# Performance work log

Measured on AMD Instinct MI355X. Metric: run time of the kernel, lower is better.

Reference implementation:

```python
import jax, jax.numpy as jnp
import numpy as np

CLASH_WEIGHT = 0.05
PHYSICS_WEIGHT = 0.3
CLAMP_DIST = 10.0
EPS = 1e-8
C_IDX, N_IDX = 0, 1  # ATOM_TYPE_MAP['C'], ATOM_TYPE_MAP['N']


def setup_inputs() -> dict:
    key = jax.random.key(0)
    ks = jax.random.split(key, 8)
    B, R, A = 2, 1024, 4096
    return {
        'rots_pred': jax.random.normal(ks[0], (B, R, 3, 3), dtype=jnp.float32),
        'trans_pred': jax.random.normal(ks[1], (B, R, 3), dtype=jnp.float32),
        'coords_pred': jax.random.normal(ks[2], (B, A, 3), dtype=jnp.float32),
        'rots_true': jax.random.normal(ks[3], (B, R, 3, 3), dtype=jnp.float32),
        'trans_true': jax.random.normal(ks[4], (B, R, 3), dtype=jnp.float32),
        'coords_true': jax.random.normal(ks[5], (B, A, 3), dtype=jnp.float32),
        'atom_types': jax.random.randint(ks[6], (B, A), 0, 19, dtype=jnp.int32),
        'vdw_radii': jax.random.uniform(ks[7], (19,), dtype=jnp.float32),
        'res_mask': jnp.ones((B, R), dtype=jnp.float32),
        'mask': jnp.ones((B, A), dtype=jnp.float32),
    }


def _local_coords(rots, trans, coords):
    # invert_frames: R^-1 = R^T, t^-1 = -R^T t ; apply to all points per frame
    inv_rots = jnp.swapaxes(rots, -1, -2)                      # [B,R,3,3]
    inv_trans = -jnp.einsum('brij,brj->bri', inv_rots, trans)  # [B,R,3]
    # [B, R, A, 3]
    return jnp.einsum('brij,baj->brai', inv_rots, coords) + inv_trans[:, :, None, :]


def _pairwise_dist(coords, eps2=1e-12):
    # numerically-stable cdist via squared-norm expansion
    sq = jnp.sum(coords * coords, axis=-1)                      # [B,A]
    d2 = sq[:, :, None] + sq[:, None, :] - 2.0 * jnp.einsum('bad,bcd->bac', coords, coords)
    return jnp.sqrt(jnp.maximum(d2, eps2))                      # [B,A,A]


def reference(rots_pred, trans_pred, coords_pred, rots_true, trans_true,
              coords_true, atom_types, vdw_radii, res_mask, mask):
    # ---- FAPE ----
    lp = _local_coords(rots_pred, trans_pred, coords_pred)   # [B,R,A,3]
    lt = _local_coords(rots_true, trans_true, coords_true)   # [B,R,A,3]
    err = jnp.sqrt(jnp.sum((lp - lt) ** 2, axis=-1) + EPS)   # [B,R,A]
    err = jnp.minimum(err, CLAMP_DIST)
    err = err * mask[:, None, :] * res_mask[:, :, None]
    fape = jnp.sum(err) / (jnp.sum(mask) * jnp.sum(res_mask) + EPS)

    # shared pairwise distances on predicted coords
    d = _pairwise_dist(coords_pred)                          # [B,A,A]

    # ---- Clash ----
    radii = vdw_radii[atom_types]                            # [B,A]
    min_d = radii[:, :, None] + radii[:, None, :]
    clashes = (d < min_d) & (d > EPS)
    num_clashes = jnp.sum(clashes.astype(jnp.float32), axis=(-1, -2)) / 2.0
    num_atoms = coords_pred.shape[-2]
    clash = jnp.mean(num_clashes / num_atoms)

    # ---- Physics (C-N peptide bond length) ----
    is_c = atom_types == C_IDX
    is_n = atom_types == N_IDX
    cn_mask = (is_c[:, :, None] & is_n[:, None, :]).astype(jnp.float32)
    penalty = jax.nn.relu(jnp.abs(d - 1.33) - 0.2) * cn_mask
    total_pen = jnp.sum(penalty, axis=(-1, -2))
    n_pairs = jnp.maximum(jnp.sum(cn_mask, axis=(-1, -2)), 1.0)
    physics = jnp.mean(total_pen / n_pairs)

    total = fape + CLASH_WEIGHT * clash + PHYSICS_WEIGHT * physics
    return total
```

## Files before the change

kernel.cpp:

```cpp
#include <hip/hip_runtime.h>


constexpr int BB = 2;
constexpr int FR = 4;
constexpr int NI = 4;
constexpr int TJ = 16;
constexpr int IC = 1024;

constexpr int NB_FAPE = 512;
constexpr int NB_BAND = 512;
constexpr int NB_FULL = 768;
constexpr int NB_PAIR = NB_BAND + NB_FULL;

__device__ __forceinline__ float wred(float v) {
#pragma unroll
  for (int o = 32; o > 0; o >>= 1) v += __shfl_down(v, o, 64);
  return v;
}
__device__ __forceinline__ double wredd(double v) {
#pragma unroll
  for (int o = 32; o > 0; o >>= 1) v += __shfl_down(v, o, 64);
  return v;
}

template <bool BAND>
__device__ __forceinline__ void pair_body(
    const float* __restrict__ coords, const int* __restrict__ types,
    const float* __restrict__ vdw, int A, int b, int ic, int jt, int tid,
    float& out_clash, float& out_pen) {
  const int ibase = ic * IC;
  float xi[NI], yi[NI], zi[NI], qi[NI], ri[NI], cf[NI], nf[NI];
  int ii[NI];
#pragma unroll
  for (int k = 0; k < NI; ++k) {
    ii[k] = ibase + (k << 8) + tid;
    const size_t g = (size_t)b * A + ii[k];
    const float x = coords[g * 3], y = coords[g * 3 + 1], z = coords[g * 3 + 2];
    const int t = types[g];
    xi[k] = x; yi[k] = y; zi[k] = z;
    qi[k] = __fadd_rn(__fadd_rn(__fmul_rn(x, x), __fmul_rn(y, y)), __fmul_rn(z, z));
    ri[k] = vdw[t];
    cf[k] = (t == 0) ? 1.f : 0.f;
    nf[k] = (t == 1) ? 1.f : 0.f;
  }

  int cnt2 = 0, cnt1 = 0;
  float pen = 0.f;
  const int j0 = jt * TJ;
#pragma unroll 4
  for (int jj = 0; jj < TJ; ++jj) {
    const int j = j0 + jj;
    const size_t jg = (size_t)b * A + j;
    const float sx = coords[jg * 3], sy = coords[jg * 3 + 1], sz = coords[jg * 3 + 2];
    const int st = types[jg];
    const float sr = vdw[st];
    const float sq = __fadd_rn(__fadd_rn(__fmul_rn(sx, sx), __fmul_rn(sy, sy)),
                               __fmul_rn(sz, sz));
    float dsq[NI];
#pragma unroll
    for (int k = 0; k < NI; ++k) {
      const float dot = fmaf(zi[k], sz, fmaf(yi[k], sy, xi[k] * sx));
      float d2 = fmaf(-2.f, dot, qi[k] + sq);
      d2 = fmaxf(d2, 1e-12f);
      dsq[k] = d2;
      const float mind = ri[k] + sr;
      const bool c = d2 < mind * mind;
      if (BAND) {
        cnt2 += (c && (ii[k] < j)) ? 1 : 0;
        cnt1 += (c && (ii[k] == j)) ? 1 : 0;
      } else {
        cnt2 += c ? 1 : 0;
      }
    }
    if (st <= 1) {
      if (st == 1) {
#pragma unroll
        for (int k = 0; k < NI; ++k) {
          const float dd = __builtin_amdgcn_sqrtf(dsq[k]);
          float pp = fmaxf(fabsf(dd - 1.33f) - 0.2f, 0.f);
          if (BAND) pp = (ii[k] < j) ? pp : 0.f;
          pen = fmaf(pp, cf[k], pen);
        }
      } else {
#pragma unroll
        for (int k = 0; k < NI; ++k) {
          const float dd = __builtin_amdgcn_sqrtf(dsq[k]);
          float pp = fmaxf(fabsf(dd - 1.33f) - 0.2f, 0.f);
          if (BAND) pp = (ii[k] < j) ? pp : 0.f;
          pen = fmaf(pp, nf[k], pen);
        }
      }
    }
  }
  out_clash = 2.f * cnt2 + (float)cnt1;
  out_pen = pen;
}

__global__ __launch_bounds__(256) void fat_kernel(
    const float* __restrict__ rots_p, const float* __restrict__ trans_p,
    const float* __restrict__ coords_p,
    const float* __restrict__ rots_t, const float* __restrict__ trans_t,
    const float* __restrict__ coords_t,
    const int* __restrict__ types, const float* __restrict__ vdw,
    const float* __restrict__ res_mask, const float* __restrict__ mask,
    float* __restrict__ fape_part, float* __restrict__ clash_part,
    float* __restrict__ pen_part, int R, int A) {
  const int tid = threadIdx.x;
  const int bid = blockIdx.x;
  __shared__ float red[2][4];

  if (bid < NB_FAPE) {
    const int bpb = R / FR;
    const int b = bid / bpb;
    const int r0 = (bid % bpb) * FR;

    float rp[FR][9], rt[FR][9], cc[FR][3], rm[FR];
#pragma unroll
    for (int f = 0; f < FR; ++f) {
      const size_t fr = (size_t)(b * R + r0 + f);
      const float* Rp = rots_p + fr * 9;
      const float* Rt = rots_t + fr * 9;
      const float* Tp = trans_p + fr * 3;
      const float* Tt = trans_t + fr * 3;
#pragma unroll
      for (int k = 0; k < 9; ++k) { rp[f][k] = Rp[k]; rt[f][k] = Rt[k]; }
      const float tp0 = Tp[0], tp1 = Tp[1], tp2 = Tp[2];
      const float tt0 = Tt[0], tt1 = Tt[1], tt2 = Tt[2];
#pragma unroll
      for (int i = 0; i < 3; ++i) {
        cc[f][i] = (rp[f][0 + i] * tp0 + rp[f][3 + i] * tp1 + rp[f][6 + i] * tp2)
                 - (rt[f][0 + i] * tt0 + rt[f][3 + i] * tt1 + rt[f][6 + i] * tt2);
      }
      rm[f] = res_mask[fr];
    }

    float facc[FR];
#pragma unroll
    for (int f = 0; f < FR; ++f) facc[f] = 0.f;

    for (int a = tid; a < A; a += 256) {
      const size_t g = (size_t)b * A + a;
      const float x0 = coords_p[g * 3], x1 = coords_p[g * 3 + 1], x2 = coords_p[g * 3 + 2];
      const float y0 = coords_t[g * 3], y1 = coords_t[g * 3 + 1], y2 = coords_t[g * 3 + 2];
      const float m = mask[g];
#pragma unroll
      for (int f = 0; f < FR; ++f) {
        float u0 = fmaf(rp[f][0], x0, -cc[f][0]);
        u0 = fmaf(rp[f][3], x1, u0); u0 = fmaf(rp[f][6], x2, u0);
        u0 = fmaf(-rt[f][0], y0, u0); u0 = fmaf(-rt[f][3], y1, u0); u0 = fmaf(-rt[f][6], y2, u0);
        float u1 = fmaf(rp[f][1], x0, -cc[f][1]);
        u1 = fmaf(rp[f][4], x1, u1); u1 = fmaf(rp[f][7], x2, u1);
        u1 = fmaf(-rt[f][1], y0, u1); u1 = fmaf(-rt[f][4], y1, u1); u1 = fmaf(-rt[f][7], y2, u1);
        float u2 = fmaf(rp[f][2], x0, -cc[f][2]);
        u2 = fmaf(rp[f][5], x1, u2); u2 = fmaf(rp[f][8], x2, u2);
        u2 = fmaf(-rt[f][2], y0, u2); u2 = fmaf(-rt[f][5], y1, u2); u2 = fmaf(-rt[f][8], y2, u2);
        float e2 = fmaf(u0, u0, 1e-8f);
        e2 = fmaf(u1, u1, e2);
        e2 = fmaf(u2, u2, e2);
        float e = __builtin_amdgcn_sqrtf(e2);
        e = fminf(e, 10.0f);
        facc[f] = fmaf(e, m, facc[f]);
      }
    }

    float tot = 0.f;
#pragma unroll
    for (int f = 0; f < FR; ++f) tot = fmaf(facc[f], rm[f], tot);

    tot = wred(tot);
    if ((tid & 63) == 0) red[0][tid >> 6] = tot;
    __syncthreads();
    if (tid == 0) fape_part[bid] = red[0][0] + red[0][1] + red[0][2] + red[0][3];
    return;
  }

  int b, ic, jt;
  bool band;
  if (bid < NB_FAPE + NB_BAND) {
    const int q = bid - NB_FAPE;
    band = true;
    b = q >> 8;
    const int r = q & 255;
    ic = r >> 6;
    jt = (ic << 6) + (r & 63);
  } else {
    const int q = bid - (NB_FAPE + NB_BAND);
    band = false;
    b = q / 384;
    const int r = q % 384;
    if (r < 192)      { ic = 0; jt = 64 + r; }
    else if (r < 320) { ic = 1; jt = 128 + (r - 192); }
    else              { ic = 2; jt = 192 + (r - 320); }
  }

  float oc, op;
  if (band) pair_body<true >(coords_p, types, vdw, A, b, ic, jt, tid, oc, op);
  else      pair_body<false>(coords_p, types, vdw, A, b, ic, jt, tid, oc, op);

  const float rc = wred(oc);
  const float rpn = wred(op);
  if ((tid & 63) == 0) { red[0][tid >> 6] = rc; red[1][tid >> 6] = rpn; }
  __syncthreads();
  if (tid == 0) {
    const int pidx = bid - NB_FAPE;
    clash_part[pidx] = red[0][0] + red[0][1] + red[0][2] + red[0][3];
    pen_part[pidx]   = red[1][0] + red[1][1] + red[1][2] + red[1][3];
  }
}

__global__ __launch_bounds__(256) void finalize_kernel(
    const int* __restrict__ types, const float* __restrict__ res_mask,
    const float* __restrict__ mask,
    const float* __restrict__ fape_part, const float* __restrict__ clash_part,
    const float* __restrict__ pen_part,
    float* __restrict__ out, int R, int A) {
  const int tid = threadIdx.x;
  double sf = 0.0, sc0 = 0.0, sc1 = 0.0, sp0 = 0.0, sp1 = 0.0;
  for (int i = tid; i < NB_FAPE; i += 256) sf += (double)fape_part[i];
  for (int p = tid; p < NB_PAIR; p += 256) {
    const int bb = (p < NB_BAND) ? (p >> 8) : ((p - NB_BAND) / 384);
    const double c = (double)clash_part[p];
    const double pe = (double)pen_part[p];
    if (bb == 0) { sc0 += c; sp0 += pe; } else { sc1 += c; sp1 += pe; }
  }
  float cc0 = 0, cn0 = 0, cc1 = 0, cn1 = 0, sm = 0, srm = 0;
  for (int a = tid; a < A; a += 256) {
    const int t0 = types[a], t1 = types[A + a];
    cc0 += (t0 == 0) ? 1.f : 0.f;
    cn0 += (t0 == 1) ? 1.f : 0.f;
    cc1 += (t1 == 0) ? 1.f : 0.f;
    cn1 += (t1 == 1) ? 1.f : 0.f;
    sm += mask[a] + mask[A + a];
  }
  for (int r = tid; r < R; r += 256) srm += res_mask[r] + res_mask[R + r];

  __shared__ double dred[5][4];
  __shared__ float fred[6][4];
  double dv[5] = {sf, sc0, sc1, sp0, sp1};
  float fv[6] = {cc0, cn0, cc1, cn1, sm, srm};
#pragma unroll
  for (int k = 0; k < 5; ++k) {
    const double v = wredd(dv[k]);
    if ((tid & 63) == 0) dred[k][tid >> 6] = v;
  }
#pragma unroll
  for (int k = 0; k < 6; ++k) {
    const float v = wred(fv[k]);
    if ((tid & 63) == 0) fred[k][tid >> 6] = v;
  }
  __syncthreads();
  if (tid == 0) {
    double D[5];
    float F[6];
#pragma unroll
    for (int k = 0; k < 5; ++k) D[k] = dred[k][0] + dred[k][1] + dred[k][2] + dred[k][3];
#pragma unroll
    for (int k = 0; k < 6; ++k) F[k] = fred[k][0] + fred[k][1] + fred[k][2] + fred[k][3];
    const double fape = D[0] / ((double)F[4] * (double)F[5] + 1e-8);
    const double clash = (D[1] + D[2]) / (4.0 * (double)A);
    const double np0 = fmax((double)F[0] * (double)F[1], 1.0);
    const double np1 = fmax((double)F[2] * (double)F[3], 1.0);
    const double phys = 0.5 * (D[3] / np0 + D[4] / np1);
    out[0] = (float)(fape + 0.05 * clash + 0.3 * phys);
  }
}

extern "C" void kernel_launch(void* const* d_in, const int* in_sizes, int n_in,
                              void* d_out, int out_size, void* d_ws, size_t ws_size,
                              hipStream_t stream) {
  const float* rots_p   = (const float*)d_in[0];
  const float* trans_p  = (const float*)d_in[1];
  const float* coords_p = (const float*)d_in[2];
  const float* rots_t   = (const float*)d_in[3];
  const float* trans_t  = (const float*)d_in[4];
  const float* coords_t = (const float*)d_in[5];
  const int*   types    = (const int*)d_in[6];
  const float* vdw      = (const float*)d_in[7];
  const float* res_mask = (const float*)d_in[8];
  const float* mask     = (const float*)d_in[9];
  float* out = (float*)d_out;

  const int R = in_sizes[8] / BB;
  const int A = in_sizes[9] / BB;

  float* fape_part  = (float*)d_ws;
  float* clash_part = fape_part + NB_FAPE;
  float* pen_part   = clash_part + NB_PAIR;

  fat_kernel<<<NB_FAPE + NB_PAIR, 256, 0, stream>>>(
      rots_p, trans_p, coords_p, rots_t, trans_t, coords_t, types, vdw,
      res_mask, mask, fape_part, clash_part, pen_part, R, A);

  finalize_kernel<<<1, 256, 0, stream>>>(
      types, res_mask, mask, fape_part, clash_part, pen_part, out, R, A);
}
```

Baseline: 96.23 us.

## Fuse finalize into main kernel via last-block atomic, restructure FAPE tiling

```diff
diff --git a/kernel.cpp b/kernel.cpp
--- a/kernel.cpp
+++ b/kernel.cpp
@@ -2,15 +2,20 @@
 
 
 constexpr int BB = 2;
-constexpr int FR = 4;
+
+constexpr int NA = 4;
+constexpr int RCH = 16;
+constexpr int NB_FAPE = 512;
+
 constexpr int NI = 4;
 constexpr int TJ = 16;
 constexpr int IC = 1024;
-
-constexpr int NB_FAPE = 512;
 constexpr int NB_BAND = 512;
 constexpr int NB_FULL = 768;
 constexpr int NB_PAIR = NB_BAND + NB_FULL;
+
+constexpr int NB_STAT = 4;
+constexpr int NB_TOT = NB_STAT + NB_FAPE + NB_PAIR;
 
 __device__ __forceinline__ float wred(float v) {
 #pragma unroll
@@ -27,7 +32,7 @@
 __device__ __forceinline__ void pair_body(
     const float* __restrict__ coords, const int* __restrict__ types,
     const float* __restrict__ vdw, int A, int b, int ic, int jt, int tid,
-    float& out_clash, float& out_pen) {
+    float& out_clash_wave, float& out_pen) {
   const int ibase = ic * IC;
   float xi[NI], yi[NI], zi[NI], qi[NI], ri[NI], cf[NI], nf[NI];
   int ii[NI];
@@ -66,33 +71,25 @@
       const float mind = ri[k] + sr;
       const bool c = d2 < mind * mind;
       if (BAND) {
-        cnt2 += (c && (ii[k] < j)) ? 1 : 0;
-        cnt1 += (c && (ii[k] == j)) ? 1 : 0;
+        cnt2 += __popcll(__ballot(c && (ii[k] < j)));
+        cnt1 += __popcll(__ballot(c && (ii[k] == j)));
       } else {
-        cnt2 += c ? 1 : 0;
+        cnt2 += __popcll(__ballot(c));
       }
     }
     if (st <= 1) {
-      if (st == 1) {
-#pragma unroll
-        for (int k = 0; k < NI; ++k) {
-          const float dd = __builtin_amdgcn_sqrtf(dsq[k]);
-          float pp = fmaxf(fabsf(dd - 1.33f) - 0.2f, 0.f);
-          if (BAND) pp = (ii[k] < j) ? pp : 0.f;
-          pen = fmaf(pp, cf[k], pen);
-        }
-      } else {
-#pragma unroll
-        for (int k = 0; k < NI; ++k) {
-          const float dd = __builtin_amdgcn_sqrtf(dsq[k]);
-          float pp = fmaxf(fabsf(dd - 1.33f) - 0.2f, 0.f);
-          if (BAND) pp = (ii[k] < j) ? pp : 0.f;
-          pen = fmaf(pp, nf[k], pen);
-        }
+      const bool jn = (st == 1);
+#pragma unroll
+      for (int k = 0; k < NI; ++k) {
+        const float dd = __builtin_amdgcn_sqrtf(dsq[k]);
+        float pp = fmaxf(fabsf(dd - 1.33f) - 0.2f, 0.f);
+        if (BAND) pp = (ii[k] < j) ? pp : 0.f;
+        const float fl = jn ? cf[k] : nf[k];
+        pen = fmaf(pp, fl, pen);
       }
     }
   }
-  out_clash = 2.f * cnt2 + (float)cnt1;
+  out_clash_wave = 2.f * cnt2 + (float)cnt1;
   out_pen = pen;
 }
 
@@ -103,163 +100,176 @@
     const float* __restrict__ coords_t,
     const int* __restrict__ types, const float* __restrict__ vdw,
     const float* __restrict__ res_mask, const float* __restrict__ mask,
-    float* __restrict__ fape_part, float* __restrict__ clash_part,
-    float* __restrict__ pen_part, int R, int A) {
+    float* __restrict__ wsf, float* __restrict__ out, int R, int A) {
   const int tid = threadIdx.x;
   const int bid = blockIdx.x;
-  __shared__ float red[2][4];
-
-  if (bid < NB_FAPE) {
-    const int bpb = R / FR;
-    const int b = bid / bpb;
-    const int r0 = (bid % bpb) * FR;
-
-    float rp[FR][9], rt[FR][9], cc[FR][3], rm[FR];
-#pragma unroll
-    for (int f = 0; f < FR; ++f) {
-      const size_t fr = (size_t)(b * R + r0 + f);
-      const float* Rp = rots_p + fr * 9;
-      const float* Rt = rots_t + fr * 9;
-      const float* Tp = trans_p + fr * 3;
-      const float* Tt = trans_t + fr * 3;
-#pragma unroll
-      for (int k = 0; k < 9; ++k) { rp[f][k] = Rp[k]; rt[f][k] = Rt[k]; }
-      const float tp0 = Tp[0], tp1 = Tp[1], tp2 = Tp[2];
-      const float tt0 = Tt[0], tt1 = Tt[1], tt2 = Tt[2];
-#pragma unroll
-      for (int i = 0; i < 3; ++i) {
-        cc[f][i] = (rp[f][0 + i] * tp0 + rp[f][3 + i] * tp1 + rp[f][6 + i] * tp2)
-                 - (rt[f][0 + i] * tt0 + rt[f][3 + i] * tt1 + rt[f][6 + i] * tt2);
-      }
-      rm[f] = res_mask[fr];
+  __shared__ float sh_f[3][4];
+  __shared__ double sh_d[5][4];
+  __shared__ int sh_last;
+
+  float* fape_part  = wsf + 4;
+  float* clash_part = wsf + 4 + NB_FAPE;
+  float* pen_part   = wsf + 4 + NB_FAPE + NB_PAIR;
+  float* stats      = wsf + 4 + NB_FAPE + 2 * NB_PAIR;
+
+  if (bid < NB_STAT) {
+    if (bid < 2) {
+      const int b = bid;
+      float c = 0.f, n = 0.f, ms = 0.f;
+      for (int a = tid; a < A; a += 256) {
+        const int t = types[(size_t)b * A + a];
+        c += (t == 0) ? 1.f : 0.f;
+        n += (t == 1) ? 1.f : 0.f;
+        ms += mask[(size_t)b * A + a];
+      }
+      c = wred(c); n = wred(n); ms = wred(ms);
+      if ((tid & 63) == 0) {
+        const int w = tid >> 6;
+        sh_f[0][w] = c; sh_f[1][w] = n; sh_f[2][w] = ms;
+      }
+      __syncthreads();
+      if (tid == 0) {
+        stats[b * 3 + 0] = sh_f[0][0] + sh_f[0][1] + sh_f[0][2] + sh_f[0][3];
+        stats[b * 3 + 1] = sh_f[1][0] + sh_f[1][1] + sh_f[1][2] + sh_f[1][3];
+        stats[b * 3 + 2] = sh_f[2][0] + sh_f[2][1] + sh_f[2][2] + sh_f[2][3];
+      }
+    } else {
+      const int b = bid - 2;
+      float rs = 0.f;
+      for (int r = tid; r < R; r += 256) rs += res_mask[(size_t)b * R + r];
+      rs = wred(rs);
+      if ((tid & 63) == 0) sh_f[0][tid >> 6] = rs;
+      __syncthreads();
+      if (tid == 0) stats[6 + b] = sh_f[0][0] + sh_f[0][1] + sh_f[0][2] + sh_f[0][3];
     }
-
-    float facc[FR];
-#pragma unroll
-    for (int f = 0; f < FR; ++f) facc[f] = 0.f;
-
-    for (int a = tid; a < A; a += 256) {
-      const size_t g = (size_t)b * A + a;
-      const float x0 = coords_p[g * 3], x1 = coords_p[g * 3 + 1], x2 = coords_p[g * 3 + 2];
-      const float y0 = coords_t[g * 3], y1 = coords_t[g * 3 + 1], y2 = coords_t[g * 3 + 2];
-      const float m = mask[g];
-#pragma unroll
-      for (int f = 0; f < FR; ++f) {
-        float u0 = fmaf(rp[f][0], x0, -cc[f][0]);
-        u0 = fmaf(rp[f][3], x1, u0); u0 = fmaf(rp[f][6], x2, u0);
-        u0 = fmaf(-rt[f][0], y0, u0); u0 = fmaf(-rt[f][3], y1, u0); u0 = fmaf(-rt[f][6], y2, u0);
-        float u1 = fmaf(rp[f][1], x0, -cc[f][1]);
-        u1 = fmaf(rp[f][4], x1, u1); u1 = fmaf(rp[f][7], x2, u1);
-        u1 = fmaf(-rt[f][1], y0, u1); u1 = fmaf(-rt[f][4], y1, u1); u1 = fmaf(-rt[f][7], y2, u1);
-        float u2 = fmaf(rp[f][2], x0, -cc[f][2]);
-        u2 = fmaf(rp[f][5], x1, u2); u2 = fmaf(rp[f][8], x2, u2);
-        u2 = fmaf(-rt[f][2], y0, u2); u2 = fmaf(-rt[f][5], y1, u2); u2 = fmaf(-rt[f][8], y2, u2);
-        float e2 = fmaf(u0, u0, 1e-8f);
-        e2 = fmaf(u1, u1, e2);
-        e2 = fmaf(u2, u2, e2);
-        float e = __builtin_amdgcn_sqrtf(e2);
-        e = fminf(e, 10.0f);
-        facc[f] = fmaf(e, m, facc[f]);
+  } else {
+    const int q = bid - NB_STAT;
+    const int g7 = q / 7, r7 = q % 7;
+    if (r7 < 2) {
+      const int fbid = g7 * 2 + r7;
+      const int ag = fbid & 7;
+      const int rc = fbid >> 3;
+      const int b = ag >> 2;
+      const int abase = ag * 1024;
+
+      float ax[NA], ay[NA], az[NA], bx[NA], by[NA], bz[NA], am[NA], acc[NA];
+#pragma unroll
+      for (int k = 0; k < NA; ++k) {
+        const size_t gx = (size_t)abase + tid + 256 * k;
+        ax[k] = coords_p[gx * 3]; ay[k] = coords_p[gx * 3 + 1]; az[k] = coords_p[gx * 3 + 2];
+        bx[k] = coords_t[gx * 3]; by[k] = coords_t[gx * 3 + 1]; bz[k] = coords_t[gx * 3 + 2];
+        am[k] = mask[gx];
+        acc[k] = 0.f;
+      }
+
+      const int fr0 = b * R + rc * RCH;
+      for (int f = 0; f < RCH; ++f) {
+        const size_t fr = (size_t)(fr0 + f);
+        const float* Rp = rots_p + fr * 9;
+        const float* Rt = rots_t + fr * 9;
+        float rp[9], rt[9];
+#pragma unroll
+        for (int k2 = 0; k2 < 9; ++k2) { rp[k2] = Rp[k2]; rt[k2] = Rt[k2]; }
+        const float tp0 = trans_p[fr * 3], tp1 = trans_p[fr * 3 + 1], tp2 = trans_p[fr * 3 + 2];
+        const float tt0 = trans_t[fr * 3], tt1 = trans_t[fr * 3 + 1], tt2 = trans_t[fr * 3 + 2];
+        const float rm = res_mask[fr];
+        float cc[3];
+#pragma unroll
+        for (int i = 0; i < 3; ++i) {
+          cc[i] = (rp[i] * tp0 + rp[3 + i] * tp1 + rp[6 + i] * tp2)
+                - (rt[i] * tt0 + rt[3 + i] * tt1 + rt[6 + i] * tt2);
+        }
+#pragma unroll
+        for (int k = 0; k < NA; ++k) {
+          float u0 = fmaf(rp[0], ax[k], -cc[0]);
+          u0 = fmaf(rp[3], ay[k], u0); u0 = fmaf(rp[6], az[k], u0);
+          u0 = fmaf(-rt[0], bx[k], u0); u0 = fmaf(-rt[3], by[k], u0); u0 = fmaf(-rt[6], bz[k], u0);
+          float u1 = fmaf(rp[1], ax[k], -cc[1]);
+          u1 = fmaf(rp[4], ay[k], u1); u1 = fmaf(rp[7], az[k], u1);
+          u1 = fmaf(-rt[1], bx[k], u1); u1 = fmaf(-rt[4], by[k], u1); u1 = fmaf(-rt[7], bz[k], u1);
+          float u2 = fmaf(rp[2], ax[k], -cc[2]);
+          u2 = fmaf(rp[5], ay[k], u2); u2 = fmaf(rp[8], az[k], u2);
+          u2 = fmaf(-rt[2], bx[k], u2); u2 = fmaf(-rt[5], by[k], u2); u2 = fmaf(-rt[8], bz[k], u2);
+          float e2 = fmaf(u0, u0, 1e-8f);
+          e2 = fmaf(u1, u1, e2);
+          e2 = fmaf(u2, u2, e2);
+          const float e = fminf(__builtin_amdgcn_sqrtf(e2), 10.f);
+          acc[k] = fmaf(e, rm, acc[k]);
+        }
+      }
+      float tot = 0.f;
+#pragma unroll
+      for (int k = 0; k < NA; ++k) tot = fmaf(acc[k], am[k], tot);
+      tot = wred(tot);
+      if ((tid & 63) == 0) sh_f[0][tid >> 6] = tot;
+      __syncthreads();
+      if (tid == 0) fape_part[fbid] = sh_f[0][0] + sh_f[0][1] + sh_f[0][2] + sh_f[0][3];
+    } else {
+      const int pbid = g7 * 5 + (r7 - 2);
+      int b, ic, jt;
+      bool band;
+      if (pbid < NB_BAND) {
+        band = true;
+        b = pbid >> 8;
+        const int r = pbid & 255;
+        ic = r >> 6;
+        jt = (ic << 6) + (r & 63);
+      } else {
+        const int q2 = pbid - NB_BAND;
+        band = false;
+        b = q2 / 384;
+        const int r = q2 % 384;
+        if (r < 192)      { ic = 0; jt = 64 + r; }
+        else if (r < 320) { ic = 1; jt = 128 + (r - 192); }
+        else              { ic = 2; jt = 192 + (r - 320); }
+      }
+      float oc, op;
+      if (band) pair_body<true >(coords_p, types, vdw, A, b, ic, jt, tid, oc, op);
+      else      pair_body<false>(coords_p, types, vdw, A, b, ic, jt, tid, oc, op);
+      const float rpn = wred(op);
+      if ((tid & 63) == 0) { sh_f[0][tid >> 6] = oc; sh_f[1][tid >> 6] = rpn; }
+      __syncthreads();
+      if (tid == 0) {
+        clash_part[pbid] = sh_f[0][0] + sh_f[0][1] + sh_f[0][2] + sh_f[0][3];
+        pen_part[pbid]   = sh_f[1][0] + sh_f[1][1] + sh_f[1][2] + sh_f[1][3];
       }
     }
-
-    float tot = 0.f;
-#pragma unroll
-    for (int f = 0; f < FR; ++f) tot = fmaf(facc[f], rm[f], tot);
-
-    tot = wred(tot);
-    if ((tid & 63) == 0) red[0][tid >> 6] = tot;
-    __syncthreads();
-    if (tid == 0) fape_part[bid] = red[0][0] + red[0][1] + red[0][2] + red[0][3];
-    return;
-  }
-
-  int b, ic, jt;
-  bool band;
-  if (bid < NB_FAPE + NB_BAND) {
-    const int q = bid - NB_FAPE;
-    band = true;
-    b = q >> 8;
-    const int r = q & 255;
-    ic = r >> 6;
-    jt = (ic << 6) + (r & 63);
-  } else {
-    const int q = bid - (NB_FAPE + NB_BAND);
-    band = false;
-    b = q / 384;
-    const int r = q % 384;
-    if (r < 192)      { ic = 0; jt = 64 + r; }
-    else if (r < 320) { ic = 1; jt = 128 + (r - 192); }
-    else              { ic = 2; jt = 192 + (r - 320); }
-  }
-
-  float oc, op;
-  if (band) pair_body<true >(coords_p, types, vdw, A, b, ic, jt, tid, oc, op);
-  else      pair_body<false>(coords_p, types, vdw, A, b, ic, jt, tid, oc, op);
-
-  const float rc = wred(oc);
-  const float rpn = wred(op);
-  if ((tid & 63) == 0) { red[0][tid >> 6] = rc; red[1][tid >> 6] = rpn; }
+  }
+
+  __threadfence();
+  if (tid == 0) {
+    const unsigned old = atomicAdd((unsigned*)wsf, 1u);
+    sh_last = (old == (unsigned)(NB_TOT - 1)) ? 1 : 0;
+  }
   __syncthreads();
-  if (tid == 0) {
-    const int pidx = bid - NB_FAPE;
-    clash_part[pidx] = red[0][0] + red[0][1] + red[0][2] + red[0][3];
-    pen_part[pidx]   = red[1][0] + red[1][1] + red[1][2] + red[1][3];
-  }
-}
-
-__global__ __launch_bounds__(256) void finalize_kernel(
-    const int* __restrict__ types, const float* __restrict__ res_mask,
-    const float* __restrict__ mask,
-    const float* __restrict__ fape_part, const float* __restrict__ clash_part,
-    const float* __restrict__ pen_part,
-    float* __restrict__ out, int R, int A) {
-  const int tid = threadIdx.x;
-  double sf = 0.0, sc0 = 0.0, sc1 = 0.0, sp0 = 0.0, sp1 = 0.0;
+  if (!sh_last) return;
+  __threadfence();
+
+  double sf = 0.0, c0 = 0.0, c1 = 0.0, p0 = 0.0, p1 = 0.0;
   for (int i = tid; i < NB_FAPE; i += 256) sf += (double)fape_part[i];
   for (int p = tid; p < NB_PAIR; p += 256) {
-    const int bb = (p < NB_BAND) ? (p >> 8) : ((p - NB_BAND) / 384);
-    const double c = (double)clash_part[p];
-    const double pe = (double)pen_part[p];
-    if (bb == 0) { sc0 += c; sp0 += pe; } else { sc1 += c; sp1 += pe; }
-  }
-  float cc0 = 0, cn0 = 0, cc1 = 0, cn1 = 0, sm = 0, srm = 0;
-  for (int a = tid; a < A; a += 256) {
-    const int t0 = types[a], t1 = types[A + a];
-    cc0 += (t0 == 0) ? 1.f : 0.f;
-    cn0 += (t0 == 1) ? 1.f : 0.f;
-    cc1 += (t1 == 0) ? 1.f : 0.f;
-    cn1 += (t1 == 1) ? 1.f : 0.f;
-    sm += mask[a] + mask[A + a];
-  }
-  for (int r = tid; r < R; r += 256) srm += res_mask[r] + res_mask[R + r];
-
-  __shared__ double dred[5][4];
-  __shared__ float fred[6][4];
-  double dv[5] = {sf, sc0, sc1, sp0, sp1};
-  float fv[6] = {cc0, cn0, cc1, cn1, sm, srm};
+    const int bb2 = (p < NB_BAND) ? (p >> 8) : ((p - NB_BAND) / 384);
+    const double cv = (double)clash_part[p];
+    const double pv = (double)pen_part[p];
+    if (bb2 == 0) { c0 += cv; p0 += pv; } else { c1 += cv; p1 += pv; }
+  }
+  double dv[5] = {sf, c0, c1, p0, p1};
 #pragma unroll
   for (int k = 0; k < 5; ++k) {
     const double v = wredd(dv[k]);
-    if ((tid & 63) == 0) dred[k][tid >> 6] = v;
-  }
-#pragma unroll
-  for (int k = 0; k < 6; ++k) {
-    const float v = wred(fv[k]);
-    if ((tid & 63) == 0) fred[k][tid >> 6] = v;
+    if ((tid & 63) == 0) sh_d[k][tid >> 6] = v;
   }
   __syncthreads();
   if (tid == 0) {
     double D[5];
-    float F[6];
-#pragma unroll
-    for (int k = 0; k < 5; ++k) D[k] = dred[k][0] + dred[k][1] + dred[k][2] + dred[k][3];
-#pragma unroll
-    for (int k = 0; k < 6; ++k) F[k] = fred[k][0] + fred[k][1] + fred[k][2] + fred[k][3];
-    const double fape = D[0] / ((double)F[4] * (double)F[5] + 1e-8);
+#pragma unroll
+    for (int k = 0; k < 5; ++k) D[k] = sh_d[k][0] + sh_d[k][1] + sh_d[k][2] + sh_d[k][3];
+    const double msum = (double)stats[2] + (double)stats[5];
+    const double rsum = (double)stats[6] + (double)stats[7];
+    const double fape = D[0] / (msum * rsum + 1e-8);
     const double clash = (D[1] + D[2]) / (4.0 * (double)A);
-    const double np0 = fmax((double)F[0] * (double)F[1], 1.0);
-    const double np1 = fmax((double)F[2] * (double)F[3], 1.0);
+    const double np0 = fmax((double)stats[0] * (double)stats[1], 1.0);
+    const double np1 = fmax((double)stats[3] * (double)stats[4], 1.0);
     const double phys = 0.5 * (D[3] / np0 + D[4] / np1);
     out[0] = (float)(fape + 0.05 * clash + 0.3 * phys);
   }
@@ -283,14 +293,8 @@
   const int R = in_sizes[8] / BB;
   const int A = in_sizes[9] / BB;
 
-  float* fape_part  = (float*)d_ws;
-  float* clash_part = fape_part + NB_FAPE;
-  float* pen_part   = clash_part + NB_PAIR;
-
-  fat_kernel<<<NB_FAPE + NB_PAIR, 256, 0, stream>>>(
+  hipMemsetAsync(d_ws, 0, 4, stream);
+  fat_kernel<<<NB_TOT, 256, 0, stream>>>(
       rots_p, trans_p, coords_p, rots_t, trans_t, coords_t, types, vdw,
-      res_mask, mask, fape_part, clash_part, pen_part, R, A);
-
-  finalize_kernel<<<1, 256, 0, stream>>>(
-      types, res_mask, mask, fape_part, clash_part, pen_part, out, R, A);
-}
+      res_mask, mask, (float*)d_ws, out, R, A);
+}
```

Measured after the change: 194.9 us. 103% more time.
